# Performance work log

Measured on AMD Instinct MI355X. Metric: run time of the kernel, lower is better.

## Reference

```python
import jax, jax.numpy as jnp
import numpy as np

DIM = 256
NUM_HEADS = 8
SCALE = (DIM // NUM_HEADS) ** (-0.5)
EPS = 1e-6


def channel_layernorm(x, w, b):
    # LayerNorm over channel dim (axis=1) per spatial location, as in source
    u = jnp.mean(x, axis=1, keepdims=True)
    s = jnp.mean((x - u) ** 2, axis=1, keepdims=True)
    xn = (x - u) / jnp.sqrt(s + EPS)
    return w[:, None, None] * xn + b[:, None, None]


def conv1x1(x, W, b):
    # x: [B,C,H,W], W: [O,C], b: [O]
    return jnp.einsum('bchw,oc->bohw', x, W) + b[:, None, None]


def setup_inputs() -> dict:
    key = jax.random.key(0)
    ks = jax.random.split(key, 10)
    B, C, H, W = 8, DIM, 48, 48
    inp = {
        'x1': jax.random.normal(ks[0], (B, C, H, W), jnp.float32),
        'x2': jax.random.normal(ks[1], (B, C, H, W), jnp.float32),
        'Wq': jax.random.normal(ks[2], (C, C), jnp.float32) * (1.0 / np.sqrt(C)),
        'bq': jnp.zeros((C,), jnp.float32),
        'Wk': jax.random.normal(ks[3], (C, C), jnp.float32) * (1.0 / np.sqrt(C)),
        'bk': jnp.zeros((C,), jnp.float32),
        'Wv': jax.random.normal(ks[4], (C, C), jnp.float32) * (1.0 / np.sqrt(C)),
        'bv': jnp.zeros((C,), jnp.float32),
        'Wp': jax.random.normal(ks[5], (C, C), jnp.float32) * (1.0 / np.sqrt(C)),
        'bp': jnp.zeros((C,), jnp.float32),
        'w_nq': jnp.ones((C,), jnp.float32),
        'b_nq': jnp.zeros((C,), jnp.float32),
        'w_nkv': jnp.ones((C,), jnp.float32),
        'b_nkv': jnp.zeros((C,), jnp.float32),
    }
    return inp


def reference(x1, x2, Wq, bq, Wk, bk, Wv, bv, Wp, bp, w_nq, b_nq, w_nkv, b_nkv):
    B, C, H, W = x1.shape
    x1n = channel_layernorm(x1, w_nq, b_nq)
    x2n = channel_layernorm(x2, w_nkv, b_nkv)
    # project then flatten spatial -> tokens: [B, N, C]
    q = conv1x1(x1n, Wq, bq).reshape(B, C, H * W).transpose(0, 2, 1)
    k = conv1x1(x2n, Wk, bk).reshape(B, C, H * W).transpose(0, 2, 1)
    v = conv1x1(x2n, Wv, bv).reshape(B, C, H * W).transpose(0, 2, 1)
    # single-head full attention over N tokens (heads never split in source)
    attn = jnp.einsum('bnc,bmc->bnm', q, k) * SCALE
    attn = jax.nn.softmax(attn, axis=-1)
    out = jnp.einsum('bnm,bmc->bnc', attn, v)  # [B,N,C]
    out = out.transpose(0, 2, 1).reshape(B, C, H, W)
    out = conv1x1(out, Wp, bp)
    return out + x1
```

## Files before the change

kernel.cpp:

```cpp
#include <hip/hip_runtime.h>

#define NB 8
#define CH 256
#define NT 2304
#define KVSPLIT 4
#define TPS 18
#define QB 128
#define QSCALE 0.2550349f
#define DEFER_THR 11.5415604f
#define LN_EPS 1e-6f

typedef __attribute__((ext_vector_type(8))) short short8;
typedef __attribute__((ext_vector_type(4))) float f32x4;
typedef __attribute__((ext_vector_type(16))) float f32x16;
typedef __attribute__((ext_vector_type(4))) unsigned short ushort4v;
typedef __attribute__((ext_vector_type(8))) unsigned short ushort8v;
typedef __attribute__((ext_vector_type(4))) float float4v;
typedef __attribute__((ext_vector_type(2))) unsigned int uint2v;

__device__ __forceinline__ unsigned short f2bf(float f) {
  unsigned int u = __float_as_uint(f);
  u += 0x7fffu + ((u >> 16) & 1u);
  return (unsigned short)(u >> 16);
}
__device__ __forceinline__ float bf2f(unsigned short s) {
  return __uint_as_float(((unsigned int)s) << 16);
}
__device__ __forceinline__ unsigned int cvtpk(float a, float b) {
  unsigned int r;
  asm("v_cvt_pk_bf16_f32 %0, %1, %2" : "=v"(r) : "v"(a), "v"(b));
  return r;
}

__device__ __forceinline__ void gload_lds16(const void* g, void* l) {
  __builtin_amdgcn_global_load_lds(
      (const __attribute__((address_space(1))) unsigned int*)g,
      (__attribute__((address_space(3))) unsigned int*)l, 16, 0, 0);
}

__global__ __launch_bounds__(256) void wconv_kernel(
    const float* __restrict__ wq, const float* __restrict__ wk,
    const float* __restrict__ wv, const float* __restrict__ wp,
    unsigned short* __restrict__ out) {
  int z = blockIdx.y;
  const float* src = (z == 0) ? wq : (z == 1) ? wk : (z == 2) ? wv : wp;
  unsigned short* dst = out + z * 65536;
  int i = (blockIdx.x * 256 + threadIdx.x) * 4;
  float4v v = *(const float4v*)(src + i);
  ushort4v r;
  r[0] = f2bf(v[0]); r[1] = f2bf(v[1]); r[2] = f2bf(v[2]); r[3] = f2bf(v[3]);
  *(ushort4v*)(dst + i) = r;
}

__global__ __launch_bounds__(256) void ln_kernel(
    const float* __restrict__ x1, const float* __restrict__ x2,
    const float* __restrict__ w1, const float* __restrict__ b1,
    const float* __restrict__ w2, const float* __restrict__ b2,
    unsigned short* __restrict__ o1, unsigned short* __restrict__ o2) {
  __shared__ float part[4][64][2];
  __shared__ float fin[64][2];
  int z = blockIdx.z;
  const float* x = z ? x2 : x1;
  const float* w = z ? w2 : w1;
  const float* bias = z ? b2 : b1;
  unsigned short* out = z ? o2 : o1;
  int tid = threadIdx.x;
  int lane = tid & 63, wv = tid >> 6;
  int n0 = blockIdx.x * 64;
  int b = blockIdx.y;
  const float* xp = x + (size_t)b * CH * NT + n0 + lane;
  float xc[64];
  float sum = 0.f, ss = 0.f;
#pragma unroll
  for (int j = 0; j < 64; ++j) {
    float v = xp[(size_t)(wv * 64 + j) * NT];
    xc[j] = v;
    sum += v; ss += v * v;
  }
  part[wv][lane][0] = sum;
  part[wv][lane][1] = ss;
  __syncthreads();
  if (tid < 64) {
    float s = 0.f, q = 0.f;
#pragma unroll
    for (int wi = 0; wi < 4; ++wi) { s += part[wi][tid][0]; q += part[wi][tid][1]; }
    float u = s * (1.0f / CH);
    float var = q * (1.0f / CH) - u * u;
    fin[tid][0] = u;
    fin[tid][1] = rsqrtf(var + LN_EPS);
  }
  __syncthreads();
  float u = fin[lane][0], rstd = fin[lane][1];
  unsigned short* op = out + ((size_t)b * NT + n0 + lane) * CH;
#pragma unroll
  for (int c0 = 0; c0 < 64; c0 += 8) {
    ushort8v pk;
#pragma unroll
    for (int j = 0; j < 8; ++j)
      pk[j] = f2bf((xc[c0 + j] - u) * rstd * w[wv * 64 + c0 + j] +
                   bias[wv * 64 + c0 + j]);
    *(ushort8v*)(op + wv * 64 + c0) = pk;
  }
}

__global__ __launch_bounds__(256) void proj_kernel(
    const unsigned short* __restrict__ xq, const unsigned short* __restrict__ xkv,
    const unsigned short* __restrict__ wbf,
    const float* __restrict__ bq, const float* __restrict__ bk,
    const float* __restrict__ bv,
    unsigned short* __restrict__ q, unsigned short* __restrict__ k,
    unsigned short* __restrict__ vt) {
  __shared__ char As[16384];
  __shared__ char Bs[16384];
  int tid = threadIdx.x;
  int lane = tid & 63, wid = tid >> 6;
  int z = blockIdx.z;
  int b = z / 3, pz = z - b * 3;
  const unsigned short* A = ((pz == 0) ? xq : xkv) + (size_t)b * NT * CH;
  const unsigned short* W = wbf + pz * 65536;
  const float* bias = (pz == 0) ? bq : (pz == 1) ? bk : bv;
  int m0 = blockIdx.x * 128;
  int c0 = blockIdx.y * 128;
  int wr = wid >> 1, wc = wid & 1;

  f32x4 zero4 = {0.f, 0.f, 0.f, 0.f};
  f32x4 acc[4][4];
#pragma unroll
  for (int i = 0; i < 4; ++i)
#pragma unroll
    for (int j = 0; j < 4; ++j) acc[i][j] = zero4;

  for (int kt = 0; kt < 4; ++kt) {
#pragma unroll
    for (int it = 0; it < 4; ++it) {
      int li = it * 256 + tid;
      int X = li * 16;
      int row = X >> 7;
      int colb = (X & 127) ^ ((row & 7) << 4);
      gload_lds16((const char*)A + ((size_t)(m0 + row) * CH + kt * 64) * 2 + colb,
                  As + it * 4096 + wid * 1024);
      gload_lds16((const char*)W + ((size_t)(c0 + row) * CH + kt * 64) * 2 + colb,
                  Bs + it * 4096 + wid * 1024);
    }
    __syncthreads();
#pragma unroll
    for (int kk = 0; kk < 2; ++kk) {
      int cb = kk * 64 + ((lane >> 4) << 4);
      short8 af[4], bf[4];
#pragma unroll
      for (int mi = 0; mi < 4; ++mi) {
        int row = wr * 64 + mi * 16 + (lane & 15);
        af[mi] = *(const short8*)(As + row * 128 + (cb ^ ((row & 7) << 4)));
      }
#pragma unroll
      for (int ni = 0; ni < 4; ++ni) {
        int row = wc * 64 + ni * 16 + (lane & 15);
        bf[ni] = *(const short8*)(Bs + row * 128 + (cb ^ ((row & 7) << 4)));
      }
#pragma unroll
      for (int mi = 0; mi < 4; ++mi)
#pragma unroll
        for (int ni = 0; ni < 4; ++ni)
          acc[mi][ni] = __builtin_amdgcn_mfma_f32_16x16x32_bf16(
              af[mi], bf[ni], acc[mi][ni], 0, 0, 0);
    }
    __syncthreads();
  }

  int colbase = c0 + wc * 64;
  int rowbase = m0 + wr * 64;
  if (pz < 2) {
    unsigned short* dst = ((pz == 0) ? q : k) + (size_t)b * NT * CH;
    float scl = (pz == 0) ? QSCALE : 1.0f;
#pragma unroll
    for (int mi = 0; mi < 4; ++mi)
#pragma unroll
      for (int ni = 0; ni < 4; ++ni) {
        int col = colbase + ni * 16 + (lane & 15);
        float bb = bias[col];
        int row0 = rowbase + mi * 16 + ((lane >> 4) << 2);
#pragma unroll
        for (int r = 0; r < 4; ++r)
          dst[(size_t)(row0 + r) * CH + col] = f2bf((acc[mi][ni][r] + bb) * scl);
      }
  } else {
    unsigned short* dst = vt + (size_t)b * CH * NT;
#pragma unroll
    for (int mi = 0; mi < 4; ++mi)
#pragma unroll
      for (int ni = 0; ni < 4; ++ni) {
        int col = colbase + ni * 16 + (lane & 15);
        float bb = bias[col];
        int row0 = rowbase + mi * 16 + ((lane >> 4) << 2);
        ushort4v pk;
#pragma unroll
        for (int r = 0; r < 4; ++r) pk[r] = f2bf(acc[mi][ni][r] + bb);
        *(ushort4v*)(dst + (size_t)col * NT + row0) = pk;
      }
  }
}

#define STAGEK(kt, buf)                                                        \
  {                                                                            \
    _Pragma("unroll") for (int it = 0; it < 4; ++it) {                         \
      int rowk = it * 8 + wid * 2 + (lane >> 5);                               \
      int colb = ((lane & 31) * 16) ^ ((rowk & 7) << 4);                       \
      gload_lds16((const char*)kb + ((size_t)((kt) + rowk) * CH) * 2 + colb,   \
                  (buf) + it * 4096 + wid * 1024);                             \
    }                                                                          \
  }
#define STAGEV(kt, buf)                                                        \
  {                                                                            \
    _Pragma("unroll") for (int it = 0; it < 4; ++it) {                         \
      int rowv = it * 64 + wid * 16 + (lane >> 2);                             \
      int sic = ((lane & 3) ^ ((lane >> 3) & 3)) << 4;                         \
      gload_lds16((const char*)vb + ((size_t)rowv * NT + (kt)) * 2 + sic,      \
                  (buf) + it * 4096 + wid * 1024);                             \
    }                                                                          \
  }

__global__ __launch_bounds__(256, 2) void attn_kernel(
    const unsigned short* __restrict__ q, const unsigned short* __restrict__ k,
    const unsigned short* __restrict__ vt,
    unsigned short* __restrict__ op0, unsigned short* __restrict__ op1,
    unsigned short* __restrict__ op2, unsigned short* __restrict__ op3,
    float* __restrict__ ml) {
  __shared__ __align__(1024) char Ks[2][16384];
  __shared__ __align__(1024) char Vs[2][16384];
  int tid = threadIdx.x, lane = tid & 63, wid = tid >> 6;
  int r31 = lane & 31, h2 = lane >> 5;
  int b = blockIdx.z;
  int split = blockIdx.y;
  int q0 = blockIdx.x * QB;
  const unsigned short* qb_ = q + (size_t)b * NT * CH;
  const unsigned short* kb = k + (size_t)b * NT * CH;
  const unsigned short* vb = vt + (size_t)b * CH * NT;

  int qrow = q0 + wid * 32 + r31;
  short8 qf[16];
#pragma unroll
  for (int st = 0; st < 16; ++st)
    qf[st] = *(const short8*)(qb_ + (size_t)qrow * CH + st * 16 + h2 * 8);

  f32x16 o[8];
#pragma unroll
  for (int i = 0; i < 8; ++i) o[i] = (f32x16){};
  float mrun = -INFINITY, lrun = 0.f;

  int kt0base = split * (TPS * 32);
  STAGEK(kt0base, Ks[0]);
  STAGEV(kt0base, Vs[0]);
  __syncthreads();

  int sw4 = (r31 & 7) << 4;
  int sw3 = (r31 & 6) << 3;
  int oj0 = (8 * h2) ^ sw3, oj1 = (8 * h2 + 16) ^ sw3;
  int oj2 = (8 * h2 + 32) ^ sw3, oj3 = (8 * h2 + 48) ^ sw3;

  union V16 { uint2v p[2]; short8 s8; };
  union PB { unsigned int u[4]; short8 s8; };

  for (int t = 0; t < TPS; ++t) {
    int kt0 = kt0base + t * 32;
    const char* kbase = Ks[t & 1] + r31 * 512 + ((h2 * 16) ^ sw4);
    const char* vL = Vs[t & 1] + r31 * 64;
    if (t + 1 < TPS) {
      STAGEK(kt0 + 32, Ks[(t + 1) & 1]);
      STAGEV(kt0 + 32, Vs[(t + 1) & 1]);
    }

    f32x16 s = (f32x16){};
    __builtin_amdgcn_s_setprio(1);
#pragma unroll
    for (int st = 0; st < 16; ++st) {
      short8 kf = *(const short8*)((unsigned long long)kbase ^ (unsigned)(st * 32));
      s = __builtin_amdgcn_mfma_f32_32x32x16_bf16(kf, qf[st], s, 0, 0, 0);
    }
    __builtin_amdgcn_s_setprio(0);

    float mx = fmaxf(s[0], s[1]);
#pragma unroll
    for (int i = 2; i < 16; ++i) mx = fmaxf(mx, s[i]);
    mx = fmaxf(mx, __shfl_xor(mx, 32));
    if (__any(mx - mrun > DEFER_THR)) {
      float mnew = fmaxf(mrun, mx);
      float al = exp2f(mrun - mnew);
      lrun *= al;
      mrun = mnew;
#pragma unroll
      for (int i = 0; i < 8; ++i) o[i] = o[i] * al;
    }
    float rs = 0.f;
#pragma unroll
    for (int i = 0; i < 16; ++i) {
      s[i] = exp2f(s[i] - mrun);
      rs += s[i];
    }
    rs += __shfl_xor(rs, 32);
    lrun += rs;

    PB pbA, pbB;
    pbA.u[0] = cvtpk(s[0], s[1]);   pbA.u[1] = cvtpk(s[2], s[3]);
    pbA.u[2] = cvtpk(s[4], s[5]);   pbA.u[3] = cvtpk(s[6], s[7]);
    pbB.u[0] = cvtpk(s[8], s[9]);   pbB.u[1] = cvtpk(s[10], s[11]);
    pbB.u[2] = cvtpk(s[12], s[13]); pbB.u[3] = cvtpk(s[14], s[15]);

    __builtin_amdgcn_s_setprio(1);
#pragma unroll
    for (int d2 = 0; d2 < 8; ++d2) {
      V16 a1, a2;
      a1.p[0] = *(const uint2v*)(vL + d2 * 2048 + oj0);
      a1.p[1] = *(const uint2v*)(vL + d2 * 2048 + oj1);
      a2.p[0] = *(const uint2v*)(vL + d2 * 2048 + oj2);
      a2.p[1] = *(const uint2v*)(vL + d2 * 2048 + oj3);
      o[d2] = __builtin_amdgcn_mfma_f32_32x32x16_bf16(a1.s8, pbA.s8, o[d2], 0, 0, 0);
      o[d2] = __builtin_amdgcn_mfma_f32_32x32x16_bf16(a2.s8, pbB.s8, o[d2], 0, 0, 0);
    }
    __builtin_amdgcn_s_setprio(0);
    __syncthreads();
  }

  unsigned short* od =
      ((split == 0) ? op0 : (split == 1) ? op1 : (split == 2) ? op2 : op3) +
      (size_t)(b * NT + qrow) * CH;
#pragma unroll
  for (int d2 = 0; d2 < 8; ++d2)
#pragma unroll
    for (int m = 0; m < 4; ++m) {
      ushort4v pk;
#pragma unroll
      for (int r = 0; r < 4; ++r) pk[r] = f2bf(o[d2][m * 4 + r]);
      *(ushort4v*)(od + d2 * 32 + m * 8 + h2 * 4) = pk;
    }
  if (lane < 32) {
    float* mlp = ml + ((size_t)(split * NB + b) * NT + q0 + wid * 32 + lane) * 2;
    mlp[0] = mrun;
    mlp[1] = lrun;
  }
}

__global__ __launch_bounds__(256) void combine_kernel(
    const unsigned short* __restrict__ op0, const unsigned short* __restrict__ op1,
    const unsigned short* __restrict__ op2, const unsigned short* __restrict__ op3,
    const float* __restrict__ ml, unsigned short* __restrict__ oa) {
  const size_t S = (size_t)NB * NT;
  int g = blockIdx.x * 8 + (threadIdx.x >> 5);
  int c = (threadIdx.x & 31) * 8;
  float m0 = ml[(size_t)g * 2], l0 = ml[(size_t)g * 2 + 1];
  float m1 = ml[(S + g) * 2], l1 = ml[(S + g) * 2 + 1];
  float m2 = ml[(2 * S + g) * 2], l2 = ml[(2 * S + g) * 2 + 1];
  float m3 = ml[(3 * S + g) * 2], l3 = ml[(3 * S + g) * 2 + 1];
  float M = fmaxf(fmaxf(m0, m1), fmaxf(m2, m3));
  float w0 = exp2f(m0 - M), w1 = exp2f(m1 - M);
  float w2 = exp2f(m2 - M), w3 = exp2f(m3 - M);
  float Li = 1.0f / (w0 * l0 + w1 * l1 + w2 * l2 + w3 * l3);
  w0 *= Li; w1 *= Li; w2 *= Li; w3 *= Li;
  ushort8v a0 = *(const ushort8v*)(op0 + (size_t)g * CH + c);
  ushort8v a1 = *(const ushort8v*)(op1 + (size_t)g * CH + c);
  ushort8v a2 = *(const ushort8v*)(op2 + (size_t)g * CH + c);
  ushort8v a3 = *(const ushort8v*)(op3 + (size_t)g * CH + c);
  ushort8v r;
#pragma unroll
  for (int j = 0; j < 8; ++j)
    r[j] = f2bf(w0 * bf2f(a0[j]) + w1 * bf2f(a1[j]) + w2 * bf2f(a2[j]) +
                w3 * bf2f(a3[j]));
  *(ushort8v*)(oa + (size_t)g * CH + c) = r;
}

__global__ __launch_bounds__(256) void oproj_kernel(
    const unsigned short* __restrict__ oa, const unsigned short* __restrict__ wp,
    const float* __restrict__ bp, const float* __restrict__ x1,
    float* __restrict__ outp) {
  __shared__ char As[16384];
  __shared__ char Bs[16384];
  int tid = threadIdx.x;
  int lane = tid & 63, wid = tid >> 6;
  int b = blockIdx.z;
  const unsigned short* A = oa + (size_t)b * NT * CH;
  int m0 = blockIdx.x * 128;
  int c0 = blockIdx.y * 128;
  int wr = wid >> 1, wc = wid & 1;

  f32x4 zero4 = {0.f, 0.f, 0.f, 0.f};
  f32x4 acc[4][4];
#pragma unroll
  for (int i = 0; i < 4; ++i)
#pragma unroll
    for (int j = 0; j < 4; ++j) acc[i][j] = zero4;

  for (int kt = 0; kt < 4; ++kt) {
#pragma unroll
    for (int it = 0; it < 4; ++it) {
      int li = it * 256 + tid;
      int X = li * 16;
      int row = X >> 7;
      int colb = (X & 127) ^ ((row & 7) << 4);
      gload_lds16((const char*)A + ((size_t)(m0 + row) * CH + kt * 64) * 2 + colb,
                  As + it * 4096 + wid * 1024);
      gload_lds16((const char*)wp + ((size_t)(c0 + row) * CH + kt * 64) * 2 + colb,
                  Bs + it * 4096 + wid * 1024);
    }
    __syncthreads();
#pragma unroll
    for (int kk = 0; kk < 2; ++kk) {
      int cb = kk * 64 + ((lane >> 4) << 4);
      short8 af[4], bf[4];
#pragma unroll
      for (int mi = 0; mi < 4; ++mi) {
        int row = wr * 64 + mi * 16 + (lane & 15);
        af[mi] = *(const short8*)(As + row * 128 + (cb ^ ((row & 7) << 4)));
      }
#pragma unroll
      for (int ni = 0; ni < 4; ++ni) {
        int row = wc * 64 + ni * 16 + (lane & 15);
        bf[ni] = *(const short8*)(Bs + row * 128 + (cb ^ ((row & 7) << 4)));
      }
#pragma unroll
      for (int mi = 0; mi < 4; ++mi)
#pragma unroll
        for (int ni = 0; ni < 4; ++ni)
          acc[mi][ni] = __builtin_amdgcn_mfma_f32_16x16x32_bf16(
              af[mi], bf[ni], acc[mi][ni], 0, 0, 0);
    }
    __syncthreads();
  }

  int colbase = c0 + wc * 64;
  int rowbase = m0 + wr * 64;
#pragma unroll
  for (int mi = 0; mi < 4; ++mi)
#pragma unroll
    for (int ni = 0; ni < 4; ++ni) {
      int col = colbase + ni * 16 + (lane & 15);
      float bb = bp[col];
      int row0 = rowbase + mi * 16 + ((lane >> 4) << 2);
      int base = (b * CH + col) * NT + row0;
      float4v xv = *(const float4v*)(x1 + base);
      float4v rs;
#pragma unroll
      for (int r = 0; r < 4; ++r) rs[r] = acc[mi][ni][r] + bb + xv[r];
      *(float4v*)(outp + base) = rs;
    }
}

extern "C" void kernel_launch(void* const* d_in, const int* in_sizes, int n_in,
                              void* d_out, int out_size, void* d_ws, size_t ws_size,
                              hipStream_t stream) {
  (void)in_sizes; (void)n_in; (void)out_size; (void)ws_size;
  const float* x1 = (const float*)d_in[0];
  const float* x2 = (const float*)d_in[1];
  const float* Wq = (const float*)d_in[2];
  const float* bq = (const float*)d_in[3];
  const float* Wk = (const float*)d_in[4];
  const float* bk = (const float*)d_in[5];
  const float* Wv = (const float*)d_in[6];
  const float* bv = (const float*)d_in[7];
  const float* Wp = (const float*)d_in[8];
  const float* bp = (const float*)d_in[9];
  const float* wnq = (const float*)d_in[10];
  const float* bnq = (const float*)d_in[11];
  const float* wnkv = (const float*)d_in[12];
  const float* bnkv = (const float*)d_in[13];
  float* outp = (float*)d_out;

  const size_t TSZ = (size_t)NB * NT * CH;
  unsigned short* xq = (unsigned short*)d_ws;
  unsigned short* xkv = xq + TSZ;
  unsigned short* qb = xkv + TSZ;
  unsigned short* kbuf = qb + TSZ;
  unsigned short* vtb = kbuf + TSZ;
  unsigned short* oab = vtb + TSZ;
  unsigned short* wbf = oab + TSZ;
  float* ml = (float*)(wbf + 4 * 65536);
  unsigned short* op3 = (unsigned short*)d_out;

  wconv_kernel<<<dim3(64, 4), dim3(256), 0, stream>>>(Wq, Wk, Wv, Wp, wbf);
  ln_kernel<<<dim3(36, 8, 2), dim3(256), 0, stream>>>(x1, x2, wnq, bnq, wnkv, bnkv,
                                                      xq, xkv);
  proj_kernel<<<dim3(18, 2, 24), dim3(256), 0, stream>>>(xq, xkv, wbf, bq, bk, bv,
                                                         qb, kbuf, vtb);
  attn_kernel<<<dim3(NT / QB, KVSPLIT, 8), dim3(256), 0, stream>>>(
      qb, kbuf, vtb, xq, xkv, oab, op3, ml);
  combine_kernel<<<dim3(NB * NT / 8), dim3(256), 0, stream>>>(xq, xkv, oab, op3,
                                                              ml, oab);
  oproj_kernel<<<dim3(18, 2, 8), dim3(256), 0, stream>>>(oab, wbf + 3 * 65536, bp,
                                                         x1, outp);
}
```

Measured before the change: 173.6 us.

## Split KV into five uneven chunks, single-buffer V, dual QK accumulators

The attention KV dimension is now split five ways instead of four, with uneven tile counts (15/15/14/14/14), and the combine kernel gains a fifth partial. V staging drops from double to single buffering, with an extra barrier before the PV MFMAs. This cuts LDS per block so more blocks can be resident, and together with the larger grid it aims for better CU occupancy and less tail. The QK product uses two independent accumulators, and the max and sum use tree reductions, to shorten dependency chains. In exchange V loads are less overlapped, each iteration adds a barrier, and the combine step does more traffic for the extra partial.

```diff
diff --git a/kernel.cpp b/kernel.cpp
--- a/kernel.cpp
+++ b/kernel.cpp
@@ -3,8 +3,7 @@
 #define NB 8
 #define CH 256
 #define NT 2304
-#define KVSPLIT 4
-#define TPS 18
+#define KVSPLIT 5
 #define QB 128
 #define QSCALE 0.2550349f
 #define DEFER_THR 11.5415604f
@@ -224,9 +223,9 @@
     const unsigned short* __restrict__ vt,
     unsigned short* __restrict__ op0, unsigned short* __restrict__ op1,
     unsigned short* __restrict__ op2, unsigned short* __restrict__ op3,
-    float* __restrict__ ml) {
+    unsigned short* __restrict__ op4, float* __restrict__ ml) {
   __shared__ __align__(1024) char Ks[2][16384];
-  __shared__ __align__(1024) char Vs[2][16384];
+  __shared__ __align__(1024) char Vs[16384];
   int tid = threadIdx.x, lane = tid & 63, wid = tid >> 6;
   int r31 = lane & 31, h2 = lane >> 5;
   int b = blockIdx.z;
@@ -236,6 +235,9 @@
   const unsigned short* kb = k + (size_t)b * NT * CH;
   const unsigned short* vb = vt + (size_t)b * CH * NT;
 
+  int ntiles = (split < 2) ? 15 : 14;
+  int kt0base = (split * 14 + ((split < 2) ? split : 2)) * 32;
+
   int qrow = q0 + wid * 32 + r31;
   short8 qf[16];
 #pragma unroll
@@ -247,9 +249,7 @@
   for (int i = 0; i < 8; ++i) o[i] = (f32x16){};
   float mrun = -INFINITY, lrun = 0.f;
 
-  int kt0base = split * (TPS * 32);
   STAGEK(kt0base, Ks[0]);
-  STAGEV(kt0base, Vs[0]);
   __syncthreads();
 
   int sw4 = (r31 & 7) << 4;
@@ -260,50 +260,66 @@
   union V16 { uint2v p[2]; short8 s8; };
   union PB { unsigned int u[4]; short8 s8; };
 
-  for (int t = 0; t < TPS; ++t) {
+  for (int t = 0; t < ntiles; ++t) {
     int kt0 = kt0base + t * 32;
     const char* kbase = Ks[t & 1] + r31 * 512 + ((h2 * 16) ^ sw4);
-    const char* vL = Vs[t & 1] + r31 * 64;
-    if (t + 1 < TPS) {
+    const char* vL = Vs + r31 * 64;
+    STAGEV(kt0, Vs);
+    if (t + 1 < ntiles) {
       STAGEK(kt0 + 32, Ks[(t + 1) & 1]);
-      STAGEV(kt0 + 32, Vs[(t + 1) & 1]);
-    }
-
-    f32x16 s = (f32x16){};
+    }
+
+    f32x16 s = (f32x16){}, s2 = (f32x16){};
     __builtin_amdgcn_s_setprio(1);
 #pragma unroll
-    for (int st = 0; st < 16; ++st) {
+    for (int st = 0; st < 8; ++st) {
       short8 kf = *(const short8*)((unsigned long long)kbase ^ (unsigned)(st * 32));
       s = __builtin_amdgcn_mfma_f32_32x32x16_bf16(kf, qf[st], s, 0, 0, 0);
+      short8 kg = *(const short8*)((unsigned long long)kbase ^
+                                   (unsigned)((st + 8) * 32));
+      s2 = __builtin_amdgcn_mfma_f32_32x32x16_bf16(kg, qf[st + 8], s2, 0, 0, 0);
     }
     __builtin_amdgcn_s_setprio(0);
-
-    float mx = fmaxf(s[0], s[1]);
-#pragma unroll
-    for (int i = 2; i < 16; ++i) mx = fmaxf(mx, s[i]);
-    mx = fmaxf(mx, __shfl_xor(mx, 32));
-    if (__any(mx - mrun > DEFER_THR)) {
-      float mnew = fmaxf(mrun, mx);
-      float al = exp2f(mrun - mnew);
-      lrun *= al;
-      mrun = mnew;
-#pragma unroll
-      for (int i = 0; i < 8; ++i) o[i] = o[i] * al;
-    }
-    float rs = 0.f;
-#pragma unroll
-    for (int i = 0; i < 16; ++i) {
-      s[i] = exp2f(s[i] - mrun);
-      rs += s[i];
-    }
-    rs += __shfl_xor(rs, 32);
-    lrun += rs;
+#pragma unroll
+    for (int i = 0; i < 16; ++i) s[i] += s2[i];
+
+    {
+      float t0 = fmaxf(s[0], s[1]), t1 = fmaxf(s[2], s[3]);
+      float t2 = fmaxf(s[4], s[5]), t3 = fmaxf(s[6], s[7]);
+      float t4 = fmaxf(s[8], s[9]), t5 = fmaxf(s[10], s[11]);
+      float t6 = fmaxf(s[12], s[13]), t7 = fmaxf(s[14], s[15]);
+      t0 = fmaxf(t0, t1); t2 = fmaxf(t2, t3); t4 = fmaxf(t4, t5);
+      t6 = fmaxf(t6, t7);
+      float mx = fmaxf(fmaxf(t0, t2), fmaxf(t4, t6));
+      mx = fmaxf(mx, __shfl_xor(mx, 32));
+      if (__any(mx - mrun > DEFER_THR)) {
+        float mnew = fmaxf(mrun, mx);
+        float al = exp2f(mrun - mnew);
+        lrun *= al;
+        mrun = mnew;
+#pragma unroll
+        for (int i = 0; i < 8; ++i) o[i] = o[i] * al;
+      }
+    }
+#pragma unroll
+    for (int i = 0; i < 16; ++i) s[i] = exp2f(s[i] - mrun);
+    {
+      float u0 = (s[0] + s[1]) + (s[2] + s[3]);
+      float u1 = (s[4] + s[5]) + (s[6] + s[7]);
+      float u2 = (s[8] + s[9]) + (s[10] + s[11]);
+      float u3 = (s[12] + s[13]) + (s[14] + s[15]);
+      float rs = (u0 + u1) + (u2 + u3);
+      rs += __shfl_xor(rs, 32);
+      lrun += rs;
+    }
 
     PB pbA, pbB;
     pbA.u[0] = cvtpk(s[0], s[1]);   pbA.u[1] = cvtpk(s[2], s[3]);
     pbA.u[2] = cvtpk(s[4], s[5]);   pbA.u[3] = cvtpk(s[6], s[7]);
     pbB.u[0] = cvtpk(s[8], s[9]);   pbB.u[1] = cvtpk(s[10], s[11]);
     pbB.u[2] = cvtpk(s[12], s[13]); pbB.u[3] = cvtpk(s[14], s[15]);
+
+    __syncthreads();
 
     __builtin_amdgcn_s_setprio(1);
 #pragma unroll
@@ -321,8 +337,8 @@
   }
 
   unsigned short* od =
-      ((split == 0) ? op0 : (split == 1) ? op1 : (split == 2) ? op2 : op3) +
-      (size_t)(b * NT + qrow) * CH;
+      ((split == 0) ? op0 : (split == 1) ? op1 : (split == 2) ? op2
+       : (split == 3) ? op3 : op4) + (size_t)(b * NT + qrow) * CH;
 #pragma unroll
   for (int d2 = 0; d2 < 8; ++d2)
 #pragma unroll
@@ -342,7 +358,8 @@
 __global__ __launch_bounds__(256) void combine_kernel(
     const unsigned short* __restrict__ op0, const unsigned short* __restrict__ op1,
     const unsigned short* __restrict__ op2, const unsigned short* __restrict__ op3,
-    const float* __restrict__ ml, unsigned short* __restrict__ oa) {
+    const unsigned short* __restrict__ op4, const float* __restrict__ ml,
+    unsigned short* __restrict__ oa) {
   const size_t S = (size_t)NB * NT;
   int g = blockIdx.x * 8 + (threadIdx.x >> 5);
   int c = (threadIdx.x & 31) * 8;
@@ -350,20 +367,22 @@
   float m1 = ml[(S + g) * 2], l1 = ml[(S + g) * 2 + 1];
   float m2 = ml[(2 * S + g) * 2], l2 = ml[(2 * S + g) * 2 + 1];
   float m3 = ml[(3 * S + g) * 2], l3 = ml[(3 * S + g) * 2 + 1];
-  float M = fmaxf(fmaxf(m0, m1), fmaxf(m2, m3));
-  float w0 = exp2f(m0 - M), w1 = exp2f(m1 - M);
-  float w2 = exp2f(m2 - M), w3 = exp2f(m3 - M);
-  float Li = 1.0f / (w0 * l0 + w1 * l1 + w2 * l2 + w3 * l3);
-  w0 *= Li; w1 *= Li; w2 *= Li; w3 *= Li;
+  float m4 = ml[(4 * S + g) * 2], l4 = ml[(4 * S + g) * 2 + 1];
+  float M = fmaxf(fmaxf(fmaxf(m0, m1), fmaxf(m2, m3)), m4);
+  float w0 = exp2f(m0 - M), w1 = exp2f(m1 - M), w2 = exp2f(m2 - M);
+  float w3 = exp2f(m3 - M), w4 = exp2f(m4 - M);
+  float Li = 1.0f / (w0 * l0 + w1 * l1 + w2 * l2 + w3 * l3 + w4 * l4);
+  w0 *= Li; w1 *= Li; w2 *= Li; w3 *= Li; w4 *= Li;
   ushort8v a0 = *(const ushort8v*)(op0 + (size_t)g * CH + c);
   ushort8v a1 = *(const ushort8v*)(op1 + (size_t)g * CH + c);
   ushort8v a2 = *(const ushort8v*)(op2 + (size_t)g * CH + c);
   ushort8v a3 = *(const ushort8v*)(op3 + (size_t)g * CH + c);
+  ushort8v a4 = *(const ushort8v*)(op4 + (size_t)g * CH + c);
   ushort8v r;
 #pragma unroll
   for (int j = 0; j < 8; ++j)
     r[j] = f2bf(w0 * bf2f(a0[j]) + w1 * bf2f(a1[j]) + w2 * bf2f(a2[j]) +
-                w3 * bf2f(a3[j]));
+                w3 * bf2f(a3[j]) + w4 * bf2f(a4[j]));
   *(ushort8v*)(oa + (size_t)g * CH + c) = r;
 }
 
@@ -473,6 +492,7 @@
   unsigned short* wbf = oab + TSZ;
   float* ml = (float*)(wbf + 4 * 65536);
   unsigned short* op3 = (unsigned short*)d_out;
+  unsigned short* op4 = op3 + TSZ;
 
   wconv_kernel<<<dim3(64, 4), dim3(256), 0, stream>>>(Wq, Wk, Wv, Wp, wbf);
   ln_kernel<<<dim3(36, 8, 2), dim3(256), 0, stream>>>(x1, x2, wnq, bnq, wnkv, bnkv,
@@ -480,9 +500,9 @@
   proj_kernel<<<dim3(18, 2, 24), dim3(256), 0, stream>>>(xq, xkv, wbf, bq, bk, bv,
                                                          qb, kbuf, vtb);
   attn_kernel<<<dim3(NT / QB, KVSPLIT, 8), dim3(256), 0, stream>>>(
-      qb, kbuf, vtb, xq, xkv, oab, op3, ml);
-  combine_kernel<<<dim3(NB * NT / 8), dim3(256), 0, stream>>>(xq, xkv, oab, op3,
-                                                              ml, oab);
-  oproj_kernel<<<dim3(18, 2, 8), dim3(256), 0, stream>>>(oab, wbf + 3 * 65536, bp,
+      qb, kbuf, vtb, xq, xkv, oab, op3, op4, ml);
+  combine_kernel<<<dim3(NB * NT / 8), dim3(256), 0, stream>>>(
+      xq, xkv, oab, op3, op4, ml, xq);
+  oproj_kernel<<<dim3(18, 2, 8), dim3(256), 0, stream>>>(xq, wbf + 3 * 65536, bp,
                                                          x1, outp);
 }
```

New measurement: 177.9 us. 1.03x slower.
